# Performance work log

Hardware: AMD Instinct MI355X
Metric: run time of the kernel (lower is better)

The kernel has to match this reference:

```python
import jax, jax.numpy as jnp
import numpy as np

N, E, L = 50000, 300000, 4
DN, DE, H, DO = 11, 3, 128, 2


def _ln(x, g, b, eps=1e-5):
    m = jnp.mean(x, axis=-1, keepdims=True)
    v = jnp.mean((x - m) ** 2, axis=-1, keepdims=True)
    return (x - m) * jax.lax.rsqrt(v + eps) * g + b


def _mlp(x, w1, b1, w2, b2, g, be):
    # Linear -> ReLU -> Linear -> LayerNorm (matches torch Sequential)
    h = jax.nn.relu(x @ w1 + b1)
    return _ln(h @ w2 + b2, g, be)


def setup_inputs() -> dict:
    key = jax.random.key(0)
    ks = iter(jax.random.split(key, 64))
    def nrm(shape, s=1.0):
        return jax.random.normal(next(ks), shape, jnp.float32) * s
    w = 0.02  # weight init scale
    inp = {
        'x': nrm((N, DN)),
        'edge_index': jax.random.randint(next(ks), (2, E), 0, N, jnp.int32),
        'edge_attr': nrm((E, DE)),
        'mean_vec_x': nrm((DN,)),
        'std_vec_x': jnp.ones((DN,), jnp.float32),
        'mean_vec_edge': nrm((DE,)),
        'std_vec_edge': jnp.ones((DE,), jnp.float32),
        # node encoder
        'ne_w1': nrm((DN, H), w), 'ne_b1': jnp.zeros((H,), jnp.float32),
        'ne_w2': nrm((H, H), w), 'ne_b2': jnp.zeros((H,), jnp.float32),
        'ne_g': jnp.ones((H,), jnp.float32), 'ne_be': jnp.zeros((H,), jnp.float32),
        # edge encoder
        'ee_w1': nrm((DE, H), w), 'ee_b1': jnp.zeros((H,), jnp.float32),
        'ee_w2': nrm((H, H), w), 'ee_b2': jnp.zeros((H,), jnp.float32),
        'ee_g': jnp.ones((H,), jnp.float32), 'ee_be': jnp.zeros((H,), jnp.float32),
        # processor edge MLPs (stacked over L layers): Linear(3H->H), Linear(H->H), LN
        'pe_w1': nrm((L, 3 * H, H), w), 'pe_b1': jnp.zeros((L, H), jnp.float32),
        'pe_w2': nrm((L, H, H), w), 'pe_b2': jnp.zeros((L, H), jnp.float32),
        'pe_g': jnp.ones((L, H), jnp.float32), 'pe_be': jnp.zeros((L, H), jnp.float32),
        # processor node MLPs: Linear(2H->H), Linear(H->H), LN
        'pn_w1': nrm((L, 2 * H, H), w), 'pn_b1': jnp.zeros((L, H), jnp.float32),
        'pn_w2': nrm((L, H, H), w), 'pn_b2': jnp.zeros((L, H), jnp.float32),
        'pn_g': jnp.ones((L, H), jnp.float32), 'pn_be': jnp.zeros((L, H), jnp.float32),
        # decoder: Linear(H->H) ReLU Linear(H->DO)
        'de_w1': nrm((H, H), w), 'de_b1': jnp.zeros((H,), jnp.float32),
        'de_w2': nrm((H, DO), w), 'de_b2': jnp.zeros((DO,), jnp.float32),
    }
    return inp


def reference(x, edge_index, edge_attr, mean_vec_x, std_vec_x, mean_vec_edge, std_vec_edge,
              ne_w1, ne_b1, ne_w2, ne_b2, ne_g, ne_be,
              ee_w1, ee_b1, ee_w2, ee_b2, ee_g, ee_be,
              pe_w1, pe_b1, pe_w2, pe_b2, pe_g, pe_be,
              pn_w1, pn_b1, pn_w2, pn_b2, pn_g, pn_be,
              de_w1, de_b1, de_w2, de_b2):
    x = (x - mean_vec_x) / std_vec_x
    e = (edge_attr - mean_vec_edge) / std_vec_edge
    x = _mlp(x, ne_w1, ne_b1, ne_w2, ne_b2, ne_g, ne_be)   # [N, H]
    e = _mlp(e, ee_w1, ee_b1, ee_w2, ee_b2, ee_g, ee_be)   # [E, H]
    row, col = edge_index[0], edge_index[1]
    for i in range(L):
        # edge update: gather endpoints, concat with edge feature, residual
        msg_in = jnp.concatenate([x[row], x[col], e], axis=-1)  # [E, 3H]
        e = e + _mlp(msg_in, pe_w1[i], pe_b1[i], pe_w2[i], pe_b2[i], pe_g[i], pe_be[i])
        # aggregate messages (= updated edge_attr) at target nodes (col), sum-aggr
        agg = jax.ops.segment_sum(e, col, num_segments=N)       # [N, H]
        node_in = jnp.concatenate([x, agg], axis=-1)             # [N, 2H]
        x = x + _mlp(node_in, pn_w1[i], pn_b1[i], pn_w2[i], pn_b2[i], pn_g[i], pn_be[i])
    return jax.nn.relu(x @ de_w1 + de_b1) @ de_w2 + de_b2       # [N, DO]
```

## Files before the change

### kernel.cpp

```cpp
#include <hip/hip_runtime.h>
#include <hip/hip_bf16.h>


#define NN 50000
#define EE 300000

typedef unsigned int u32;
typedef unsigned short u16;
typedef __attribute__((ext_vector_type(8))) short bf16x8;
typedef __attribute__((ext_vector_type(4))) float f32x4;

__device__ __forceinline__ float bf2f(u16 v){ return __uint_as_float(((u32)v) << 16); }
__device__ __forceinline__ u16 f2bf(float f){
  u32 u = __float_as_uint(f);
  return (u16)((u + 0x7fffu + ((u >> 16) & 1u)) >> 16);
}
#define MFMA __builtin_amdgcn_mfma_f32_16x16x32_bf16

struct CD { const void* src; float* dst; int n; };
struct IngestArgs { CD d[34]; };

__global__ __launch_bounds__(256)
void ingest_kernel(IngestArgs a, const u32* __restrict__ probe) {
  const bool isbf = (probe[0] == 0x3F803F80u);
  const CD c = a.d[blockIdx.y];
  for (int i = blockIdx.x*256 + threadIdx.x; i < c.n; i += gridDim.x*256) {
    c.dst[i] = isbf ? bf2f(((const u16*)c.src)[i]) : ((const float*)c.src)[i];
  }
}

struct PackDesc { const float* src; u16* dst; int K; int Ksrc; };
struct PackArgs { PackDesc d[20]; };

__global__ __launch_bounds__(256)
void pack_b_kernel(PackArgs pa) {
  const PackDesc p = pa.d[blockIdx.y];
  const int total = (p.K >> 5) * 512;
  for (int idx = blockIdx.x*256 + threadIdx.x; idx < total; idx += gridDim.x*256) {
    const int lane = idx & 63;
    const int tile = idx >> 6;
    const int nt = tile & 7, kt = tile >> 3;
    const int col = nt*16 + (lane & 15);
    const int k0  = kt*32 + (lane >> 4) * 8;
    u32 w4[4];
    #pragma unroll
    for (int jj = 0; jj < 4; ++jj) {
      const int ka = k0 + 2*jj, kb = k0 + 2*jj + 1;
      const u16 lo = (ka < p.Ksrc) ? f2bf(p.src[(size_t)ka * 128 + col]) : (u16)0;
      const u16 hi = (kb < p.Ksrc) ? f2bf(p.src[(size_t)kb * 128 + col]) : (u16)0;
      w4[jj] = (u32)lo | ((u32)hi << 16);
    }
    *(uint4*)(p.dst + (size_t)idx * 8) = make_uint4(w4[0], w4[1], w4[2], w4[3]);
  }
}

__global__ __launch_bounds__(256)
void zero_kernel(int4* __restrict__ p, int n4) {
  for (int i = blockIdx.x*256 + threadIdx.x; i < n4; i += gridDim.x*256)
    p[i] = make_int4(0, 0, 0, 0);
}

__global__ __launch_bounds__(256)
void hist_kernel(const int* __restrict__ ei, int* __restrict__ deg) {
  for (int i = blockIdx.x*256 + threadIdx.x; i < EE; i += gridDim.x*256)
    atomicAdd(&deg[ei[EE + i]], 1);
}

__global__ __launch_bounds__(1024)
void scan_kernel(const int* __restrict__ deg, int* __restrict__ start,
                 int* __restrict__ cursor) {
  __shared__ int sums[1024];
  const int t = threadIdx.x;
  const int base = t * 49;
  int s = 0;
  for (int j = 0; j < 49; ++j) { const int i = base + j; if (i < NN) s += deg[i]; }
  sums[t] = s; __syncthreads();
  for (int off = 1; off < 1024; off <<= 1) {
    int v = (t >= off) ? sums[t - off] : 0;
    __syncthreads();
    sums[t] += v;
    __syncthreads();
  }
  int ex = (t == 0) ? 0 : sums[t - 1];
  for (int j = 0; j < 49; ++j) {
    const int i = base + j;
    if (i < NN) { start[i] = ex; cursor[i] = ex; ex += deg[i]; }
  }
  if (t == 1023) start[NN] = ex;
}

__global__ __launch_bounds__(256)
void scatter_kernel(const int* __restrict__ ei, int* __restrict__ cursor,
                    int* __restrict__ perm, int* __restrict__ src_p,
                    int* __restrict__ dst_p) {
  for (int i = blockIdx.x*256 + threadIdx.x; i < EE; i += gridDim.x*256) {
    const int c = ei[EE + i];
    const int pos = atomicAdd(&cursor[c], 1);
    perm[pos]  = i;
    src_p[pos] = ei[i];
    dst_p[pos] = c;
  }
}

template<int KIN, int MODE>
__global__ __launch_bounds__(256)
void enc_mfma(const u16* __restrict__ w1pk, const float* __restrict__ b1,
              const u16* __restrict__ w2pk, const float* __restrict__ b2,
              const float* __restrict__ g,  const float* __restrict__ be,
              const float* __restrict__ raw, const float* __restrict__ mean,
              const float* __restrict__ stdv, const int* __restrict__ perm,
              float* __restrict__ x, u16* __restrict__ outb, int nrows)
{
  constexpr int STR = 296;
  __shared__ u16 As[64 * STR];
  const int lane  = threadIdx.x & 63;
  const int wv    = threadIdx.x >> 6;
  const int col_l = lane & 15;
  const int quad  = lane >> 4;
  const int m0    = wv * 16;
  const int r0    = blockIdx.x * 64;

  for (int t = lane; t < 256; t += 64)
    ((u32*)As)[(m0 + (t >> 4)) * 148 + (t & 15)] = 0u;
  for (int t = lane; t < 16 * KIN; t += 64) {
    const int r = t / KIN, k = t - r * KIN;
    int srow = min(r0 + m0 + r, nrows - 1);
    if constexpr (MODE == 1) srow = perm[srow];
    const float v = (raw[(size_t)srow * KIN + k] - mean[k]) / stdv[k];
    As[(m0 + r) * STR + k] = f2bf(v);
  }

  float b1v[8], b2v[8], gv[8], bev[8];
  #pragma unroll
  for (int nt = 0; nt < 8; ++nt) {
    b1v[nt] = b1[nt*16 + col_l]; b2v[nt] = b2[nt*16 + col_l];
    gv[nt]  = g [nt*16 + col_l]; bev[nt] = be[nt*16 + col_l];
  }

  const f32x4 zf = {0.f, 0.f, 0.f, 0.f};
  const bf16x8* bq1 = (const bf16x8*)w1pk;
  const bf16x8* bq2 = (const bf16x8*)w2pk;
  const u16* arow = As + (size_t)(m0 + col_l) * STR + quad * 8;

  f32x4 acc[8];
  #pragma unroll
  for (int nt = 0; nt < 8; ++nt) acc[nt] = zf;
  {
    const bf16x8 af = *(const bf16x8*)(arow);
    #pragma unroll
    for (int nt = 0; nt < 8; ++nt)
      acc[nt] = MFMA(af, bq1[nt*64 + lane], acc[nt], 0, 0, 0);
  }
  #pragma unroll
  for (int nt = 0; nt < 8; ++nt) {
    #pragma unroll
    for (int rg = 0; rg < 4; ++rg) {
      const float hv = fmaxf(acc[nt][rg] + b1v[nt], 0.f);
      As[(size_t)(m0 + quad*4 + rg) * STR + 32 + nt*16 + col_l] = f2bf(hv);
    }
  }
  f32x4 acc2[8];
  #pragma unroll
  for (int nt = 0; nt < 8; ++nt) acc2[nt] = zf;
  #pragma unroll
  for (int kt = 0; kt < 4; ++kt) {
    const bf16x8 af = *(const bf16x8*)(arow + 32 + kt * 32);
    #pragma unroll
    for (int nt = 0; nt < 8; ++nt)
      acc2[nt] = MFMA(af, bq2[(kt*8+nt)*64 + lane], acc2[nt], 0, 0, 0);
  }
  #pragma unroll
  for (int rg = 0; rg < 4; ++rg) {
    float v[8];
    float s1 = 0.f, s2 = 0.f;
    #pragma unroll
    for (int nt = 0; nt < 8; ++nt) {
      v[nt] = acc2[nt][rg] + b2v[nt];
      s1 += v[nt]; s2 += v[nt]*v[nt];
    }
    #pragma unroll
    for (int off = 1; off < 16; off <<= 1) {
      s1 += __shfl_xor(s1, off);
      s2 += __shfl_xor(s2, off);
    }
    const float mu   = s1 * (1.f/128.f);
    const float var  = s2 * (1.f/128.f) - mu*mu;
    const float rstd = rsqrtf(var + 1e-5f);
    const int rloc = m0 + quad*4 + rg;
    const int row  = r0 + rloc;
    #pragma unroll
    for (int nt = 0; nt < 8; ++nt) {
      const float y = (v[nt] - mu) * rstd * gv[nt] + bev[nt];
      As[(size_t)rloc * STR + 160 + nt*16 + col_l] = f2bf(y);
      if (MODE == 0 && row < nrows) x[(size_t)row*128 + nt*16 + col_l] = y;
    }
  }
  #pragma unroll
  for (int r = 0; r < 16; ++r) {
    const int row = r0 + m0 + r;
    if (row < nrows)
      ((u32*)(outb + (size_t)row * 128))[lane] =
          ((const u32*)(As + (size_t)(m0 + r) * STR + 160))[lane];
  }
}

__global__ __launch_bounds__(512, 2)
void edge_mfma(const u16* __restrict__ w1pk, const float* __restrict__ b1,
               const u16* __restrict__ w2pk, const float* __restrict__ b2,
               const float* __restrict__ g, const float* __restrict__ be,
               const u16* __restrict__ xb, u16* __restrict__ eb,
               const int* __restrict__ src_p, const int* __restrict__ dst_p)
{
  extern __shared__ u16 lds[];
  u16* lw1 = lds;
  u16* lw2 = lds + 49152;
  u16* lh  = lds + 65536;

  const int lane = threadIdx.x & 63;
  const int wv   = threadIdx.x >> 6;
  const int m    = lane & 15;
  const int q    = lane >> 4;
  const int rbase = wv * 16;

  for (int i = threadIdx.x; i < 6144; i += 512)
    ((uint4*)lw1)[i] = ((const uint4*)w1pk)[i];
  for (int i = threadIdx.x; i < 2048; i += 512)
    ((uint4*)lw2)[i] = ((const uint4*)w2pk)[i];

  float b1v[8], b2v[8], gv[8], bev[8];
  #pragma unroll
  for (int nt = 0; nt < 8; ++nt) {
    b1v[nt] = b1[nt*16 + m]; b2v[nt] = b2[nt*16 + m];
    gv[nt]  = g [nt*16 + m]; bev[nt] = be[nt*16 + m];
  }
  __syncthreads();

  const int ntiles = (EE + 127) >> 7;
  bf16x8 A[12];

  auto loadA = [&](int t) {
    const int grow = min(t*128 + rbase + m, EE-1);
    const u16* p0 = xb + (size_t)src_p[grow] * 128 + q*8;
    const u16* p1 = xb + (size_t)dst_p[grow] * 128 + q*8;
    const u16* p2 = eb + (size_t)grow * 128 + q*8;
    #pragma unroll
    for (int kt = 0; kt < 4; ++kt) {
      A[kt]   = *(const bf16x8*)(p0 + kt*32);
      A[4+kt] = *(const bf16x8*)(p1 + kt*32);
      A[8+kt] = *(const bf16x8*)(p2 + kt*32);
    }
  };

  loadA(blockIdx.x);
  for (int t = blockIdx.x; t < ntiles; t += 256) {
    #pragma unroll
    for (int nt = 0; nt < 8; ++nt) {
      f32x4 c = {0.f,0.f,0.f,0.f};
      #pragma unroll
      for (int kt = 0; kt < 12; ++kt) {
        const bf16x8 bf = *(const bf16x8*)(lw1 + (size_t)(kt*8+nt)*512 + lane*8);
        c = MFMA(A[kt], bf, c, 0, 0, 0);
      }
      #pragma unroll
      for (int rg = 0; rg < 4; ++rg) {
        const float hv = fmaxf(c[rg] + b1v[nt], 0.f);
        const int row = rbase + q*4 + rg;
        const int col = nt*16 + m;
        lh[row*128 + (((col>>3) ^ (row&7))<<3) + (col&7)] = f2bf(hv);
      }
    }
    const int tn = t + 256;
    if (tn < ntiles) loadA(tn);
    f32x4 acc2[8];
    #pragma unroll
    for (int nt = 0; nt < 8; ++nt) acc2[nt] = {0.f,0.f,0.f,0.f};
    #pragma unroll
    for (int kt2 = 0; kt2 < 4; ++kt2) {
      const int ra = rbase + m;
      const bf16x8 h0 = *(const bf16x8*)(lh + ra*128 + (((kt2*4+q) ^ (ra&7))<<3));
      #pragma unroll
      for (int nt = 0; nt < 8; ++nt) {
        const bf16x8 bf = *(const bf16x8*)(lw2 + (size_t)(kt2*8+nt)*512 + lane*8);
        acc2[nt] = MFMA(h0, bf, acc2[nt], 0, 0, 0);
      }
    }
    #pragma unroll
    for (int rg = 0; rg < 4; ++rg) {
      const int rloc = q*4 + rg;
      const int grow = min(t*128 + rbase + rloc, EE-1);
      float v[8]; float s1 = 0.f, s2 = 0.f;
      #pragma unroll
      for (int nt = 0; nt < 8; ++nt) {
        v[nt] = acc2[nt][rg] + b2v[nt];
        s1 += v[nt]; s2 += v[nt]*v[nt];
      }
      #pragma unroll
      for (int off = 1; off < 16; off <<= 1) {
        s1 += __shfl_xor(s1, off);
        s2 += __shfl_xor(s2, off);
      }
      const float mu   = s1 * (1.f/128.f);
      const float rstd = rsqrtf(s2*(1.f/128.f) - mu*mu + 1e-5f);
      #pragma unroll
      for (int nt = 0; nt < 8; ++nt) {
        const float y  = (v[nt] - mu) * rstd * gv[nt] + bev[nt];
        const float eo = bf2f(eb[(size_t)grow*128 + nt*16 + m]);
        const int row = rbase + rloc;
        const int col = nt*16 + m;
        lh[row*128 + (((col>>3) ^ (row&7))<<3) + (col&7)] = f2bf(y + eo);
      }
    }
    #pragma unroll
    for (int r = 0; r < 16; ++r) {
      const int grow = t*128 + rbase + r;
      if (grow < EE) {
        const int ch = (lane >> 2) ^ (r & 7);
        ((u32*)(eb + (size_t)grow * 128))[lane] =
            *(const u32*)(lh + (rbase + r)*128 + (ch<<3) + 2*(lane & 3));
      }
    }
  }
}

__global__ __launch_bounds__(512, 2)
void node_mfma(const u16* __restrict__ w1pk, const float* __restrict__ b1,
               const u16* __restrict__ w2pk, const float* __restrict__ b2,
               const float* __restrict__ g, const float* __restrict__ be,
               float* __restrict__ x, u16* __restrict__ xb,
               const u16* __restrict__ eb, const int* __restrict__ start)
{
  extern __shared__ u16 lds[];
  u16* lw1 = lds;
  u16* lw2 = lds + 32768;
  u16* lh  = lds + 49152;
  u16* lag = lds + 65536;

  const int lane = threadIdx.x & 63;
  const int wv   = threadIdx.x >> 6;
  const int m    = lane & 15;
  const int q    = lane >> 4;
  const int rbase = wv * 16;

  for (int i = threadIdx.x; i < 4096; i += 512)
    ((uint4*)lw1)[i] = ((const uint4*)w1pk)[i];
  for (int i = threadIdx.x; i < 2048; i += 512)
    ((uint4*)lw2)[i] = ((const uint4*)w2pk)[i];

  float b1v[8], b2v[8], gv[8], bev[8];
  #pragma unroll
  for (int nt = 0; nt < 8; ++nt) {
    b1v[nt] = b1[nt*16 + m]; b2v[nt] = b2[nt*16 + m];
    gv[nt]  = g [nt*16 + m]; bev[nt] = be[nt*16 + m];
  }
  __syncthreads();

  const int ntiles = (NN + 127) >> 7;
  for (int t = blockIdx.x; t < ntiles; t += 256) {
    const int gbase = t*128 + rbase;
    const int sv = start[min(gbase + (lane & 31), NN)];
    for (int r = 0; r < 16; ++r) {
      const int s0 = __shfl(sv, r), s1 = __shfl(sv, r + 1);
      float a0 = 0.f, a1 = 0.f;
      int j = s0;
      for (; j + 4 <= s1; j += 4) {
        const u32 q0 = ((const u32*)(eb + (size_t)(j  ) * 128))[lane];
        const u32 q1 = ((const u32*)(eb + (size_t)(j+1) * 128))[lane];
        const u32 q2 = ((const u32*)(eb + (size_t)(j+2) * 128))[lane];
        const u32 q3 = ((const u32*)(eb + (size_t)(j+3) * 128))[lane];
        a0 += bf2f((u16)q0) + bf2f((u16)q1) + bf2f((u16)q2) + bf2f((u16)q3);
        a1 += bf2f((u16)(q0>>16)) + bf2f((u16)(q1>>16)) + bf2f((u16)(q2>>16)) + bf2f((u16)(q3>>16));
      }
      for (; j < s1; ++j) {
        const u32 qq = ((const u32*)(eb + (size_t)j * 128))[lane];
        a0 += bf2f((u16)qq); a1 += bf2f((u16)(qq>>16));
      }
      const int lr = rbase + r;
      const int ch = (lane >> 2) ^ (r & 7);
      *(u32*)(lag + lr*128 + (ch<<3) + 2*(lane & 3)) =
          (u32)f2bf(a0) | ((u32)f2bf(a1) << 16);
    }
    bf16x8 A[8];
    {
      const int grow = min(gbase + m, NN-1);
      const u16* p0 = xb + (size_t)grow * 128 + q*8;
      const int lr = rbase + m;
      #pragma unroll
      for (int kt = 0; kt < 4; ++kt) {
        A[kt]   = *(const bf16x8*)(p0 + kt*32);
        A[4+kt] = *(const bf16x8*)(lag + lr*128 + (((kt*4+q) ^ (m&7))<<3));
      }
    }
    #pragma unroll
    for (int nt = 0; nt < 8; ++nt) {
      f32x4 c = {0.f,0.f,0.f,0.f};
      #pragma unroll
      for (int kt = 0; kt < 8; ++kt) {
        const bf16x8 bf = *(const bf16x8*)(lw1 + (size_t)(kt*8+nt)*512 + lane*8);
        c = MFMA(A[kt], bf, c, 0, 0, 0);
      }
      #pragma unroll
      for (int rg = 0; rg < 4; ++rg) {
        const float hv = fmaxf(c[rg] + b1v[nt], 0.f);
        const int row = rbase + q*4 + rg;
        const int col = nt*16 + m;
        lh[row*128 + (((col>>3) ^ (row&7))<<3) + (col&7)] = f2bf(hv);
      }
    }
    f32x4 acc2[8];
    #pragma unroll
    for (int nt = 0; nt < 8; ++nt) acc2[nt] = {0.f,0.f,0.f,0.f};
    #pragma unroll
    for (int kt2 = 0; kt2 < 4; ++kt2) {
      const int ra = rbase + m;
      const bf16x8 h0 = *(const bf16x8*)(lh + ra*128 + (((kt2*4+q) ^ (ra&7))<<3));
      #pragma unroll
      for (int nt = 0; nt < 8; ++nt) {
        const bf16x8 bf = *(const bf16x8*)(lw2 + (size_t)(kt2*8+nt)*512 + lane*8);
        acc2[nt] = MFMA(h0, bf, acc2[nt], 0, 0, 0);
      }
    }
    #pragma unroll
    for (int rg = 0; rg < 4; ++rg) {
      const int rloc = q*4 + rg;
      const int grow = t*128 + rbase + rloc;
      const int growc = min(grow, NN-1);
      float v[8]; float s1 = 0.f, s2 = 0.f;
      #pragma unroll
      for (int nt = 0; nt < 8; ++nt) {
        v[nt] = acc2[nt][rg] + b2v[nt];
        s1 += v[nt]; s2 += v[nt]*v[nt];
      }
      #pragma unroll
      for (int off = 1; off < 16; off <<= 1) {
        s1 += __shfl_xor(s1, off);
        s2 += __shfl_xor(s2, off);
      }
      const float mu   = s1 * (1.f/128.f);
      const float rstd = rsqrtf(s2*(1.f/128.f) - mu*mu + 1e-5f);
      #pragma unroll
      for (int nt = 0; nt < 8; ++nt) {
        const float y  = (v[nt] - mu) * rstd * gv[nt] + bev[nt];
        const float xn = y + x[(size_t)growc*128 + nt*16 + m];
        if (grow < NN) x[(size_t)grow*128 + nt*16 + m] = xn;
        const int row = rbase + rloc;
        const int col = nt*16 + m;
        lh[row*128 + (((col>>3) ^ (row&7))<<3) + (col&7)] = f2bf(xn);
      }
    }
    #pragma unroll
    for (int r = 0; r < 16; ++r) {
      const int grow = t*128 + rbase + r;
      if (grow < NN) {
        const int ch = (lane >> 2) ^ (r & 7);
        ((u32*)(xb + (size_t)grow * 128))[lane] =
            *(const u32*)(lh + (rbase + r)*128 + (ch<<3) + 2*(lane & 3));
      }
    }
  }
}

constexpr int TM  = 8;
constexpr int WPB = 2;

__global__ __launch_bounds__(WPB*64)
void decoder_kernel(const float* __restrict__ x,
                    const float* __restrict__ w1, const float* __restrict__ b1,
                    const float* __restrict__ w2, const float* __restrict__ b2,
                    void* __restrict__ out, const u32* __restrict__ probe,
                    int nrows)
{
  const bool isbf = (probe[0] == 0x3F803F80u);
  const int lane = threadIdx.x & 63;
  const int wv   = threadIdx.x >> 6;
  const int wgl  = blockIdx.x * WPB + wv;
  const int nw   = gridDim.x * WPB;
  extern __shared__ float smem[];
  float* in_s = smem + wv * (TM * 128);

  const float2* w1p = ((const float2*)w1) + lane;
  const float b1l = b1[2*lane], b1h = b1[2*lane+1];
  const float2 wA = ((const float2*)w2)[2*lane];
  const float2 wB = ((const float2*)w2)[2*lane+1];
  const float c0 = b2[0], c1 = b2[1];

  for (int r0 = wgl * TM; r0 < nrows; r0 += nw * TM) {
    const int rcnt = min(TM, nrows - r0);
    for (int t = lane; t < rcnt * 128; t += 64) {
      const int r = t >> 7, k = t & 127;
      in_s[r*128 + k] = x[(size_t)(r0+r)*128 + k];
    }
    float a0[TM], a1[TM];
    #pragma unroll
    for (int r=0;r<TM;++r){ a0[r]=0.f; a1[r]=0.f; }
    for (int k = 0; k < 128; k += 2) {
      const float2 wa = w1p[(k  )*64];
      const float2 wb = w1p[(k+1)*64];
      #pragma unroll
      for (int r=0;r<TM;++r){
        const float2 av = *(const float2*)(in_s + r*128 + k);
        a0[r] = fmaf(av.x, wa.x, a0[r]); a1[r] = fmaf(av.x, wa.y, a1[r]);
        a0[r] = fmaf(av.y, wb.x, a0[r]); a1[r] = fmaf(av.y, wb.y, a1[r]);
      }
    }
    for (int r = 0; r < rcnt; ++r) {
      const float h0 = fmaxf(a0[r] + b1l, 0.f);
      const float h1 = fmaxf(a1[r] + b1h, 0.f);
      float p0 = fmaf(h0, wA.x, h1 * wB.x);
      float p1 = fmaf(h0, wA.y, h1 * wB.y);
      #pragma unroll
      for (int off = 32; off; off >>= 1) {
        p0 += __shfl_xor(p0, off);
        p1 += __shfl_xor(p1, off);
      }
      if (lane == 0) {
        const float o0 = p0 + c0;
        const float o1 = p1 + c1;
        if (isbf) ((u32*)out)[r0 + r] = (u32)f2bf(o0) | ((u32)f2bf(o1) << 16);
        else      *(float2*)((float*)out + (size_t)(r0 + r)*2) = make_float2(o0, o1);
      }
    }
  }
}

extern "C" void kernel_launch(void* const* d_in, const int* in_sizes, int n_in,
                              void* d_out, int out_size, void* d_ws, size_t ws_size,
                              hipStream_t stream) {
  static const int src_idx[34] = {0,2,3,4,5,6,
    7,8,9,10,11,12, 13,14,15,16,17,18,
    19,20,21,22,23,24, 25,26,27,28,29,30, 31,32,33,34};
  static const int sz[34] = {550000,900000,11,11,3,3,
    1408,128,16384,128,128,128,
    384,128,16384,128,128,128,
    196608,512,65536,512,512,512,
    131072,512,65536,512,512,512,
    16384,128,256,2};

  IngestArgs ia;
  const float* cp[35] = {};
  float* w = (float*)d_ws;
  for (int j = 0; j < 34; ++j) {
    ia.d[j].src = d_in[src_idx[j]];
    ia.d[j].dst = w;
    ia.d[j].n   = sz[j];
    cp[src_idx[j]] = w;
    w += sz[j];
  }
  w = (float*)(((uintptr_t)w + 63) & ~(uintptr_t)63);
  float* x   = w;
  u16*   xb  = (u16*)(x + (size_t)NN*128);
  u16*   e   = xb + (size_t)NN*128;
  u16*   pk  = e  + (size_t)EE*128;
  u16* pk_pe1 = pk;
  u16* pk_pe2 = pk_pe1 + (size_t)4*384*128;
  u16* pk_pn1 = pk_pe2 + (size_t)4*128*128;
  u16* pk_pn2 = pk_pn1 + (size_t)4*256*128;
  u16* pk_ne1 = pk_pn2 + (size_t)4*128*128;
  u16* pk_ne2 = pk_ne1 + (size_t)32*128;
  u16* pk_ee1 = pk_ne2 + (size_t)128*128;
  u16* pk_ee2 = pk_ee1 + (size_t)32*128;
  int* deg    = (int*)(pk_ee2 + (size_t)128*128);
  int* start  = deg + NN;
  int* cursor = start + NN + 1;
  int* perm   = cursor + NN;
  int* src_p  = perm + EE;
  int* dst_p  = src_p + EE;

  const u32* probe = (const u32*)d_in[4];
  const int* ei    = (const int*)d_in[1];

  hipFuncSetAttribute((const void*)edge_mfma,
                      hipFuncAttributeMaxDynamicSharedMemorySize, 163840);
  hipFuncSetAttribute((const void*)node_mfma,
                      hipFuncAttributeMaxDynamicSharedMemorySize, 163840);

  ingest_kernel<<<dim3(128, 34), 256, 0, stream>>>(ia, probe);

  PackArgs pa;
  for (int l = 0; l < 4; ++l) {
    pa.d[l*4+0] = { cp[19] + (size_t)l*384*128, pk_pe1 + (size_t)l*384*128, 384, 384 };
    pa.d[l*4+1] = { cp[21] + (size_t)l*128*128, pk_pe2 + (size_t)l*128*128, 128, 128 };
    pa.d[l*4+2] = { cp[25] + (size_t)l*256*128, pk_pn1 + (size_t)l*256*128, 256, 256 };
    pa.d[l*4+3] = { cp[27] + (size_t)l*128*128, pk_pn2 + (size_t)l*128*128, 128, 128 };
  }
  pa.d[16] = { cp[7],  pk_ne1,  32,  11 };
  pa.d[17] = { cp[9],  pk_ne2, 128, 128 };
  pa.d[18] = { cp[13], pk_ee1,  32,   3 };
  pa.d[19] = { cp[15], pk_ee2, 128, 128 };
  pack_b_kernel<<<dim3(24, 20), 256, 0, stream>>>(pa);

  zero_kernel<<<dim3(64), 256, 0, stream>>>((int4*)deg, NN/4);
  hist_kernel<<<dim3(512), 256, 0, stream>>>(ei, deg);
  scan_kernel<<<dim3(1), 1024, 0, stream>>>(deg, start, cursor);
  scatter_kernel<<<dim3(512), 256, 0, stream>>>(ei, cursor, perm, src_p, dst_p);

  enc_mfma<11, 0><<<dim3((NN + 63)/64), 256, 0, stream>>>(
      pk_ne1, cp[8], pk_ne2, cp[10], cp[11], cp[12],
      cp[0], cp[3], cp[4], nullptr, x, xb, NN);
  enc_mfma<3, 1><<<dim3((EE + 63)/64), 256, 0, stream>>>(
      pk_ee1, cp[14], pk_ee2, cp[16], cp[17], cp[18],
      cp[2], cp[5], cp[6], perm, nullptr, e, EE);

  for (int l = 0; l < 4; ++l) {
    edge_mfma<<<dim3(256), dim3(512), 163840, stream>>>(
        pk_pe1 + (size_t)l*384*128, cp[20] + l*128,
        pk_pe2 + (size_t)l*128*128, cp[22] + l*128,
        cp[23] + l*128, cp[24] + l*128,
        xb, e, src_p, dst_p);
    node_mfma<<<dim3(256), dim3(512), 163840, stream>>>(
        pk_pn1 + (size_t)l*256*128, cp[26] + l*128,
        pk_pn2 + (size_t)l*128*128, cp[28] + l*128,
        cp[29] + l*128, cp[30] + l*128,
        x, xb, e, start);
  }

  decoder_kernel<<<dim3((NN + TM*WPB - 1)/(TM*WPB)), dim3(WPB*64),
                   (size_t)(WPB*TM*128*4), stream>>>(
      x, cp[31], cp[32], cp[33], cp[34], d_out, probe, NN);
}
```

Before: 1.149 ms.

## Double-buffer edge tile loads and halve node tiles to eight rows per wave

The edge MLP kernel now holds two register buffers of gathered A operands and alternates tiles, so the next tile's gathers are issued before the current tile's compute. The residual edge read moves into the coalesced write-back loop, replacing the scattered per-element reads. The node kernel processes eight real rows per wave (64 per block) with padded MFMA rows, which doubles tile count to spread segment-sum work across more blocks, at the cost of half-wasted MFMA work and higher register pressure from the doubled A buffer.

```diff
diff --git a/kernel.cpp b/kernel.cpp
--- a/kernel.cpp
+++ b/kernel.cpp
@@ -236,30 +236,29 @@
   __syncthreads();
 
   const int ntiles = (EE + 127) >> 7;
-  bf16x8 A[12];
-
-  auto loadA = [&](int t) {
+  bf16x8 A[2][12];
+
+  auto loadA = [&](int t, int b) {
     const int grow = min(t*128 + rbase + m, EE-1);
     const u16* p0 = xb + (size_t)src_p[grow] * 128 + q*8;
     const u16* p1 = xb + (size_t)dst_p[grow] * 128 + q*8;
     const u16* p2 = eb + (size_t)grow * 128 + q*8;
     #pragma unroll
     for (int kt = 0; kt < 4; ++kt) {
-      A[kt]   = *(const bf16x8*)(p0 + kt*32);
-      A[4+kt] = *(const bf16x8*)(p1 + kt*32);
-      A[8+kt] = *(const bf16x8*)(p2 + kt*32);
+      A[b][kt]   = *(const bf16x8*)(p0 + kt*32);
+      A[b][4+kt] = *(const bf16x8*)(p1 + kt*32);
+      A[b][8+kt] = *(const bf16x8*)(p2 + kt*32);
     }
   };
 
-  loadA(blockIdx.x);
-  for (int t = blockIdx.x; t < ntiles; t += 256) {
+  auto compute = [&](int t, int b) {
     #pragma unroll
     for (int nt = 0; nt < 8; ++nt) {
       f32x4 c = {0.f,0.f,0.f,0.f};
       #pragma unroll
       for (int kt = 0; kt < 12; ++kt) {
         const bf16x8 bf = *(const bf16x8*)(lw1 + (size_t)(kt*8+nt)*512 + lane*8);
-        c = MFMA(A[kt], bf, c, 0, 0, 0);
+        c = MFMA(A[b][kt], bf, c, 0, 0, 0);
       }
       #pragma unroll
       for (int rg = 0; rg < 4; ++rg) {
@@ -269,8 +268,6 @@
         lh[row*128 + (((col>>3) ^ (row&7))<<3) + (col&7)] = f2bf(hv);
       }
     }
-    const int tn = t + 256;
-    if (tn < ntiles) loadA(tn);
     f32x4 acc2[8];
     #pragma unroll
     for (int nt = 0; nt < 8; ++nt) acc2[nt] = {0.f,0.f,0.f,0.f};
@@ -287,7 +284,6 @@
     #pragma unroll
     for (int rg = 0; rg < 4; ++rg) {
       const int rloc = q*4 + rg;
-      const int grow = min(t*128 + rbase + rloc, EE-1);
       float v[8]; float s1 = 0.f, s2 = 0.f;
       #pragma unroll
       for (int nt = 0; nt < 8; ++nt) {
@@ -303,21 +299,33 @@
       const float rstd = rsqrtf(s2*(1.f/128.f) - mu*mu + 1e-5f);
       #pragma unroll
       for (int nt = 0; nt < 8; ++nt) {
-        const float y  = (v[nt] - mu) * rstd * gv[nt] + bev[nt];
-        const float eo = bf2f(eb[(size_t)grow*128 + nt*16 + m]);
+        const float y = (v[nt] - mu) * rstd * gv[nt] + bev[nt];
         const int row = rbase + rloc;
         const int col = nt*16 + m;
-        lh[row*128 + (((col>>3) ^ (row&7))<<3) + (col&7)] = f2bf(y + eo);
+        lh[row*128 + (((col>>3) ^ (row&7))<<3) + (col&7)] = f2bf(y);
       }
     }
     #pragma unroll
     for (int r = 0; r < 16; ++r) {
       const int grow = t*128 + rbase + r;
       if (grow < EE) {
+        const u32 eo = ((const u32*)(eb + (size_t)grow * 128))[lane];
         const int ch = (lane >> 2) ^ (r & 7);
-        ((u32*)(eb + (size_t)grow * 128))[lane] =
-            *(const u32*)(lh + (rbase + r)*128 + (ch<<3) + 2*(lane & 3));
-      }
+        const u32 yv = *(const u32*)(lh + (rbase + r)*128 + (ch<<3) + 2*(lane & 3));
+        const float lo = bf2f((u16)eo) + bf2f((u16)yv);
+        const float hi = bf2f((u16)(eo >> 16)) + bf2f((u16)(yv >> 16));
+        ((u32*)(eb + (size_t)grow * 128))[lane] = (u32)f2bf(lo) | ((u32)f2bf(hi) << 16);
+      }
+    }
+  };
+
+  loadA(blockIdx.x, 0);
+  for (int t = blockIdx.x; t < ntiles; t += 512) {
+    if (t + 256 < ntiles) loadA(t + 256, 1);
+    compute(t, 0);
+    if (t + 256 < ntiles) {
+      if (t + 512 < ntiles) loadA(t + 512, 0);
+      compute(t + 256, 1);
     }
   }
 }
@@ -339,7 +347,7 @@
   const int wv   = threadIdx.x >> 6;
   const int m    = lane & 15;
   const int q    = lane >> 4;
-  const int rbase = wv * 16;
+  const int rl0  = wv * 16;
 
   for (int i = threadIdx.x; i < 4096; i += 512)
     ((uint4*)lw1)[i] = ((const uint4*)w1pk)[i];
@@ -354,11 +362,11 @@
   }
   __syncthreads();
 
-  const int ntiles = (NN + 127) >> 7;
+  const int ntiles = (NN + 63) >> 6;
   for (int t = blockIdx.x; t < ntiles; t += 256) {
-    const int gbase = t*128 + rbase;
-    const int sv = start[min(gbase + (lane & 31), NN)];
-    for (int r = 0; r < 16; ++r) {
+    const int gbase = t*64 + wv*8;
+    const int sv = start[min(gbase + (lane & 15), NN)];
+    for (int r = 0; r < 8; ++r) {
       const int s0 = __shfl(sv, r), s1 = __shfl(sv, r + 1);
       float a0 = 0.f, a1 = 0.f;
       int j = s0;
@@ -374,16 +382,16 @@
         const u32 qq = ((const u32*)(eb + (size_t)j * 128))[lane];
         a0 += bf2f((u16)qq); a1 += bf2f((u16)(qq>>16));
       }
-      const int lr = rbase + r;
+      const int lr = rl0 + r;
       const int ch = (lane >> 2) ^ (r & 7);
       *(u32*)(lag + lr*128 + (ch<<3) + 2*(lane & 3)) =
           (u32)f2bf(a0) | ((u32)f2bf(a1) << 16);
     }
     bf16x8 A[8];
     {
-      const int grow = min(gbase + m, NN-1);
+      const int grow = min(gbase + (m & 7), NN-1);
       const u16* p0 = xb + (size_t)grow * 128 + q*8;
-      const int lr = rbase + m;
+      const int lr = rl0 + m;
       #pragma unroll
       for (int kt = 0; kt < 4; ++kt) {
         A[kt]   = *(const bf16x8*)(p0 + kt*32);
@@ -401,7 +409,7 @@
       #pragma unroll
       for (int rg = 0; rg < 4; ++rg) {
         const float hv = fmaxf(c[rg] + b1v[nt], 0.f);
-        const int row = rbase + q*4 + rg;
+        const int row = rl0 + q*4 + rg;
         const int col = nt*16 + m;
         lh[row*128 + (((col>>3) ^ (row&7))<<3) + (col&7)] = f2bf(hv);
       }
@@ -411,7 +419,7 @@
     for (int nt = 0; nt < 8; ++nt) acc2[nt] = {0.f,0.f,0.f,0.f};
     #pragma unroll
     for (int kt2 = 0; kt2 < 4; ++kt2) {
-      const int ra = rbase + m;
+      const int ra = rl0 + m;
       const bf16x8 h0 = *(const bf16x8*)(lh + ra*128 + (((kt2*4+q) ^ (ra&7))<<3));
       #pragma unroll
       for (int nt = 0; nt < 8; ++nt) {
@@ -422,8 +430,8 @@
     #pragma unroll
     for (int rg = 0; rg < 4; ++rg) {
       const int rloc = q*4 + rg;
-      const int grow = t*128 + rbase + rloc;
-      const int growc = min(grow, NN-1);
+      const int grow = t*64 + wv*8 + rloc;
+      const int growc = min(min(grow, t*64 + wv*8 + 7), NN-1);
       float v[8]; float s1 = 0.f, s2 = 0.f;
       #pragma unroll
       for (int nt = 0; nt < 8; ++nt) {
@@ -437,23 +445,24 @@
       }
       const float mu   = s1 * (1.f/128.f);
       const float rstd = rsqrtf(s2*(1.f/128.f) - mu*mu + 1e-5f);
+      const bool real = (rloc < 8) && (grow < NN);
       #pragma unroll
       for (int nt = 0; nt < 8; ++nt) {
         const float y  = (v[nt] - mu) * rstd * gv[nt] + bev[nt];
         const float xn = y + x[(size_t)growc*128 + nt*16 + m];
-        if (grow < NN) x[(size_t)grow*128 + nt*16 + m] = xn;
-        const int row = rbase + rloc;
+        if (real) x[(size_t)grow*128 + nt*16 + m] = xn;
+        const int row = rl0 + rloc;
         const int col = nt*16 + m;
         lh[row*128 + (((col>>3) ^ (row&7))<<3) + (col&7)] = f2bf(xn);
       }
     }
     #pragma unroll
-    for (int r = 0; r < 16; ++r) {
-      const int grow = t*128 + rbase + r;
+    for (int r = 0; r < 8; ++r) {
+      const int grow = t*64 + wv*8 + r;
       if (grow < NN) {
         const int ch = (lane >> 2) ^ (r & 7);
         ((u32*)(xb + (size_t)grow * 128))[lane] =
-            *(const u32*)(lh + (rbase + r)*128 + (ch<<3) + 2*(lane & 3));
+            *(const u32*)(lh + (rl0 + r)*128 + (ch<<3) + 2*(lane & 3));
       }
     }
   }
```

After: 1.229 ms. 1.07x slower.

## Stream edge-MLP first-layer weights through double-buffered LDS to raise occupancy

Applied to the files above, without the earlier changes.

The edge kernel no longer keeps the full W1 and W2 resident in LDS. W1 is now streamed in four K-chunks through two small LDS buffers, with a barrier per chunk, and W2 plus the bias and LayerNorm vectors are read straight from global/L2. LDS drops to 80 KB and the grid doubles to 512 blocks with a launch bound of 4, so more waves can hide the gather latency. In exchange it adds per-tile barriers and repeated weight reloads from L2, and the residual add now happens at bf16 precision during the store.

```diff
diff --git a/kernel.cpp b/kernel.cpp
--- a/kernel.cpp
+++ b/kernel.cpp
@@ -204,7 +204,7 @@
   }
 }
 
-__global__ __launch_bounds__(512, 2)
+__global__ __launch_bounds__(512, 4)
 void edge_mfma(const u16* __restrict__ w1pk, const float* __restrict__ b1,
                const u16* __restrict__ w2pk, const float* __restrict__ b2,
                const float* __restrict__ g, const float* __restrict__ be,
@@ -212,28 +212,16 @@
                const int* __restrict__ src_p, const int* __restrict__ dst_p)
 {
   extern __shared__ u16 lds[];
-  u16* lw1 = lds;
-  u16* lw2 = lds + 49152;
-  u16* lh  = lds + 65536;
-
-  const int lane = threadIdx.x & 63;
-  const int wv   = threadIdx.x >> 6;
+  u16* wbuf0 = lds;
+  u16* wbuf1 = lds + 12288;
+  u16* lh    = lds + 24576;
+
+  const int tid  = threadIdx.x;
+  const int lane = tid & 63;
+  const int wv   = tid >> 6;
   const int m    = lane & 15;
   const int q    = lane >> 4;
   const int rbase = wv * 16;
-
-  for (int i = threadIdx.x; i < 6144; i += 512)
-    ((uint4*)lw1)[i] = ((const uint4*)w1pk)[i];
-  for (int i = threadIdx.x; i < 2048; i += 512)
-    ((uint4*)lw2)[i] = ((const uint4*)w2pk)[i];
-
-  float b1v[8], b2v[8], gv[8], bev[8];
-  #pragma unroll
-  for (int nt = 0; nt < 8; ++nt) {
-    b1v[nt] = b1[nt*16 + m]; b2v[nt] = b2[nt*16 + m];
-    gv[nt]  = g [nt*16 + m]; bev[nt] = be[nt*16 + m];
-  }
-  __syncthreads();
 
   const int ntiles = (EE + 127) >> 7;
   bf16x8 A[12];
@@ -251,47 +239,72 @@
     }
   };
 
+  {
+    const uint4* s = (const uint4*)w1pk;
+    uint4* d = (uint4*)wbuf0;
+    d[tid] = s[tid]; d[tid+512] = s[tid+512]; d[tid+1024] = s[tid+1024];
+  }
   loadA(blockIdx.x);
-  for (int t = blockIdx.x; t < ntiles; t += 256) {
+  __syncthreads();
+
+  for (int t = blockIdx.x; t < ntiles; t += 512) {
+    f32x4 c[8];
+    #pragma unroll
+    for (int nt = 0; nt < 8; ++nt) c[nt] = {0.f,0.f,0.f,0.f};
+    #pragma unroll
+    for (int ks = 0; ks < 4; ++ks) {
+      uint4 nx0, nx1, nx2;
+      {
+        const uint4* s = (const uint4*)w1pk + ((ks + 1) & 3) * 1536;
+        nx0 = s[tid]; nx1 = s[tid+512]; nx2 = s[tid+1024];
+      }
+      const u16* wb = (ks & 1) ? wbuf1 : wbuf0;
+      #pragma unroll
+      for (int nt = 0; nt < 8; ++nt) {
+        #pragma unroll
+        for (int ktl = 0; ktl < 3; ++ktl) {
+          const bf16x8 bf = *(const bf16x8*)(wb + (size_t)(ktl*8+nt)*512 + lane*8);
+          c[nt] = MFMA(A[ks*3+ktl], bf, c[nt], 0, 0, 0);
+        }
+      }
+      {
+        uint4* d = (uint4*)(((ks + 1) & 1) ? wbuf1 : wbuf0);
+        d[tid] = nx0; d[tid+512] = nx1; d[tid+1024] = nx2;
+      }
+      __syncthreads();
+    }
     #pragma unroll
     for (int nt = 0; nt < 8; ++nt) {
-      f32x4 c = {0.f,0.f,0.f,0.f};
-      #pragma unroll
-      for (int kt = 0; kt < 12; ++kt) {
-        const bf16x8 bf = *(const bf16x8*)(lw1 + (size_t)(kt*8+nt)*512 + lane*8);
-        c = MFMA(A[kt], bf, c, 0, 0, 0);
-      }
+      const float b1n = b1[nt*16 + m];
       #pragma unroll
       for (int rg = 0; rg < 4; ++rg) {
-        const float hv = fmaxf(c[rg] + b1v[nt], 0.f);
+        const float hv = fmaxf(c[nt][rg] + b1n, 0.f);
         const int row = rbase + q*4 + rg;
         const int col = nt*16 + m;
         lh[row*128 + (((col>>3) ^ (row&7))<<3) + (col&7)] = f2bf(hv);
       }
     }
-    const int tn = t + 256;
-    if (tn < ntiles) loadA(tn);
-    f32x4 acc2[8];
-    #pragma unroll
-    for (int nt = 0; nt < 8; ++nt) acc2[nt] = {0.f,0.f,0.f,0.f};
+    if (t + 512 < ntiles) loadA(t + 512);
+    f32x4 a2[8];
+    #pragma unroll
+    for (int nt = 0; nt < 8; ++nt) a2[nt] = {0.f,0.f,0.f,0.f};
     #pragma unroll
     for (int kt2 = 0; kt2 < 4; ++kt2) {
       const int ra = rbase + m;
       const bf16x8 h0 = *(const bf16x8*)(lh + ra*128 + (((kt2*4+q) ^ (ra&7))<<3));
       #pragma unroll
       for (int nt = 0; nt < 8; ++nt) {
-        const bf16x8 bf = *(const bf16x8*)(lw2 + (size_t)(kt2*8+nt)*512 + lane*8);
-        acc2[nt] = MFMA(h0, bf, acc2[nt], 0, 0, 0);
+        const bf16x8 bf = ((const bf16x8*)w2pk)[(kt2*8+nt)*64 + lane];
+        a2[nt] = MFMA(h0, bf, a2[nt], 0, 0, 0);
       }
     }
     #pragma unroll
     for (int rg = 0; rg < 4; ++rg) {
       const int rloc = q*4 + rg;
-      const int grow = min(t*128 + rbase + rloc, EE-1);
       float v[8]; float s1 = 0.f, s2 = 0.f;
       #pragma unroll
       for (int nt = 0; nt < 8; ++nt) {
-        v[nt] = acc2[nt][rg] + b2v[nt];
+        v[nt] = a2[nt][rg] + b2[nt*16 + m];
         s1 += v[nt]; s2 += v[nt]*v[nt];
       }
       #pragma unroll
@@ -303,20 +316,22 @@
       const float rstd = rsqrtf(s2*(1.f/128.f) - mu*mu + 1e-5f);
       #pragma unroll
       for (int nt = 0; nt < 8; ++nt) {
-        const float y  = (v[nt] - mu) * rstd * gv[nt] + bev[nt];
-        const float eo = bf2f(eb[(size_t)grow*128 + nt*16 + m]);
+        const float y = (v[nt] - mu) * rstd * g[nt*16 + m] + be[nt*16 + m];
         const int row = rbase + rloc;
         const int col = nt*16 + m;
-        lh[row*128 + (((col>>3) ^ (row&7))<<3) + (col&7)] = f2bf(y + eo);
+        lh[row*128 + (((col>>3) ^ (row&7))<<3) + (col&7)] = f2bf(y);
       }
     }
     #pragma unroll
     for (int r = 0; r < 16; ++r) {
       const int grow = t*128 + rbase + r;
       if (grow < EE) {
+        const u32 eo = ((const u32*)(eb + (size_t)grow * 128))[lane];
         const int ch = (lane >> 2) ^ (r & 7);
-        ((u32*)(eb + (size_t)grow * 128))[lane] =
-            *(const u32*)(lh + (rbase + r)*128 + (ch<<3) + 2*(lane & 3));
+        const u32 yv = *(const u32*)(lh + (rbase + r)*128 + (ch<<3) + 2*(lane & 3));
+        const float lo = bf2f((u16)eo) + bf2f((u16)yv);
+        const float hi = bf2f((u16)(eo >> 16)) + bf2f((u16)(yv >> 16));
+        ((u32*)(eb + (size_t)grow * 128))[lane] = (u32)f2bf(lo) | ((u32)f2bf(hi) << 16);
       }
     }
   }
@@ -569,7 +584,7 @@
   const int* ei    = (const int*)d_in[1];
 
   hipFuncSetAttribute((const void*)edge_mfma,
-                      hipFuncAttributeMaxDynamicSharedMemorySize, 163840);
+                      hipFuncAttributeMaxDynamicSharedMemorySize, 81920);
   hipFuncSetAttribute((const void*)node_mfma,
                       hipFuncAttributeMaxDynamicSharedMemorySize, 163840);
 
@@ -601,7 +616,7 @@
       cp[2], cp[5], cp[6], perm, nullptr, e, EE);
 
   for (int l = 0; l < 4; ++l) {
-    edge_mfma<<<dim3(256), dim3(512), 163840, stream>>>(
+    edge_mfma<<<dim3(512), dim3(512), 81920, stream>>>(
         pk_pe1 + (size_t)l*384*128, cp[20] + l*128,
         pk_pe2 + (size_t)l*128*128, cp[22] + l*128,
         cp[23] + l*128, cp[24] + l*128,
```

Result: slower. 2.770 ms (+141.0%).

## Process two 16-row halves per wave in edge MLP to reuse weight loads

Applied to the files above, without the earlier changes.

The edge MLP kernel now handles 256 edges per tile (32 rows per wave) instead of 128. Each LDS weight fragment of the first layer feeds two MFMAs, halving LDS weight reads per edge and exposing independent MFMA chains. The second half's hidden activations stay in registers while the first half runs through layer 2 and LayerNorm in the shared LDS buffer. The residual add is moved into a coalesced read-modify-write of the edge row. The cost is much higher register pressure (two A fragment sets for prefetch plus h1v), which may lower occupancy or cause spills.

```diff
diff --git a/kernel.cpp b/kernel.cpp
--- a/kernel.cpp
+++ b/kernel.cpp
@@ -235,89 +235,117 @@
   }
   __syncthreads();
 
-  const int ntiles = (EE + 127) >> 7;
-  bf16x8 A[12];
+  const int ntiles = (EE + 255) >> 8;
+  bf16x8 A[2][12];
 
   auto loadA = [&](int t) {
-    const int grow = min(t*128 + rbase + m, EE-1);
-    const u16* p0 = xb + (size_t)src_p[grow] * 128 + q*8;
-    const u16* p1 = xb + (size_t)dst_p[grow] * 128 + q*8;
-    const u16* p2 = eb + (size_t)grow * 128 + q*8;
-    #pragma unroll
-    for (int kt = 0; kt < 4; ++kt) {
-      A[kt]   = *(const bf16x8*)(p0 + kt*32);
-      A[4+kt] = *(const bf16x8*)(p1 + kt*32);
-      A[8+kt] = *(const bf16x8*)(p2 + kt*32);
+    #pragma unroll
+    for (int h = 0; h < 2; ++h) {
+      const int grow = min(t*256 + wv*32 + h*16 + m, EE-1);
+      const u16* p0 = xb + (size_t)src_p[grow] * 128 + q*8;
+      const u16* p1 = xb + (size_t)dst_p[grow] * 128 + q*8;
+      const u16* p2 = eb + (size_t)grow * 128 + q*8;
+      #pragma unroll
+      for (int kt = 0; kt < 4; ++kt) {
+        A[h][kt]   = *(const bf16x8*)(p0 + kt*32);
+        A[h][4+kt] = *(const bf16x8*)(p1 + kt*32);
+        A[h][8+kt] = *(const bf16x8*)(p2 + kt*32);
+      }
+    }
+  };
+
+  auto tail_half = [&](f32x4* a2, int gbase) {
+    #pragma unroll
+    for (int kt2 = 0; kt2 < 4; ++kt2) {
+      const int ra = rbase + m;
+      const bf16x8 h0 = *(const bf16x8*)(lh + ra*128 + (((kt2*4+q) ^ (ra&7))<<3));
+      #pragma unroll
+      for (int nt = 0; nt < 8; ++nt) {
+        const bf16x8 bf = *(const bf16x8*)(lw2 + (size_t)(kt2*8+nt)*512 + lane*8);
+        a2[nt] = MFMA(h0, bf, a2[nt], 0, 0, 0);
+      }
+    }
+    #pragma unroll
+    for (int rg = 0; rg < 4; ++rg) {
+      const int rloc = q*4 + rg;
+      float v[8]; float s1 = 0.f, s2 = 0.f;
+      #pragma unroll
+      for (int nt = 0; nt < 8; ++nt) {
+        v[nt] = a2[nt][rg] + b2v[nt];
+        s1 += v[nt]; s2 += v[nt]*v[nt];
+      }
+      #pragma unroll
+      for (int off = 1; off < 16; off <<= 1) {
+        s1 += __shfl_xor(s1, off);
+        s2 += __shfl_xor(s2, off);
+      }
+      const float mu   = s1 * (1.f/128.f);
+      const float rstd = rsqrtf(s2*(1.f/128.f) - mu*mu + 1e-5f);
+      #pragma unroll
+      for (int nt = 0; nt < 8; ++nt) {
+        const float y = (v[nt] - mu) * rstd * gv[nt] + bev[nt];
+        const int row = rbase + rloc;
+        const int col = nt*16 + m;
+        lh[row*128 + (((col>>3) ^ (row&7))<<3) + (col&7)] = f2bf(y);
+      }
+    }
+    #pragma unroll
+    for (int r = 0; r < 16; ++r) {
+      const int grow = gbase + r;
+      if (grow < EE) {
+        const u32 eo = ((const u32*)(eb + (size_t)grow * 128))[lane];
+        const int ch = (lane >> 2) ^ (r & 7);
+        const u32 yv = *(const u32*)(lh + (rbase + r)*128 + (ch<<3) + 2*(lane & 3));
+        const float lo = bf2f((u16)eo) + bf2f((u16)yv);
+        const float hi = bf2f((u16)(eo >> 16)) + bf2f((u16)(yv >> 16));
+        ((u32*)(eb + (size_t)grow * 128))[lane] = (u32)f2bf(lo) | ((u32)f2bf(hi) << 16);
+      }
     }
   };
 
   loadA(blockIdx.x);
   for (int t = blockIdx.x; t < ntiles; t += 256) {
+    const int gbase = t*256 + wv*32;
+    float h1v[8][4];
     #pragma unroll
     for (int nt = 0; nt < 8; ++nt) {
-      f32x4 c = {0.f,0.f,0.f,0.f};
+      f32x4 c0 = {0.f,0.f,0.f,0.f}, c1 = {0.f,0.f,0.f,0.f};
       #pragma unroll
       for (int kt = 0; kt < 12; ++kt) {
         const bf16x8 bf = *(const bf16x8*)(lw1 + (size_t)(kt*8+nt)*512 + lane*8);
-        c = MFMA(A[kt], bf, c, 0, 0, 0);
+        c0 = MFMA(A[0][kt], bf, c0, 0, 0, 0);
+        c1 = MFMA(A[1][kt], bf, c1, 0, 0, 0);
       }
       #pragma unroll
       for (int rg = 0; rg < 4; ++rg) {
-        const float hv = fmaxf(c[rg] + b1v[nt], 0.f);
+        const float hv = fmaxf(c0[rg] + b1v[nt], 0.f);
         const int row = rbase + q*4 + rg;
         const int col = nt*16 + m;
         lh[row*128 + (((col>>3) ^ (row&7))<<3) + (col&7)] = f2bf(hv);
-      }
-    }
-    const int tn = t + 256;
-    if (tn < ntiles) loadA(tn);
-    f32x4 acc2[8];
-    #pragma unroll
-    for (int nt = 0; nt < 8; ++nt) acc2[nt] = {0.f,0.f,0.f,0.f};
-    #pragma unroll
-    for (int kt2 = 0; kt2 < 4; ++kt2) {
-      const int ra = rbase + m;
-      const bf16x8 h0 = *(const bf16x8*)(lh + ra*128 + (((kt2*4+q) ^ (ra&7))<<3));
-      #pragma unroll
-      for (int nt = 0; nt < 8; ++nt) {
-        const bf16x8 bf = *(const bf16x8*)(lw2 + (size_t)(kt2*8+nt)*512 + lane*8);
-        acc2[nt] = MFMA(h0, bf, acc2[nt], 0, 0, 0);
-      }
-    }
-    #pragma unroll
-    for (int rg = 0; rg < 4; ++rg) {
-      const int rloc = q*4 + rg;
-      const int grow = min(t*128 + rbase + rloc, EE-1);
-      float v[8]; float s1 = 0.f, s2 = 0.f;
-      #pragma unroll
-      for (int nt = 0; nt < 8; ++nt) {
-        v[nt] = acc2[nt][rg] + b2v[nt];
-        s1 += v[nt]; s2 += v[nt]*v[nt];
-      }
-      #pragma unroll
-      for (int off = 1; off < 16; off <<= 1) {
-        s1 += __shfl_xor(s1, off);
-        s2 += __shfl_xor(s2, off);
-      }
-      const float mu   = s1 * (1.f/128.f);
-      const float rstd = rsqrtf(s2*(1.f/128.f) - mu*mu + 1e-5f);
-      #pragma unroll
-      for (int nt = 0; nt < 8; ++nt) {
-        const float y  = (v[nt] - mu) * rstd * gv[nt] + bev[nt];
-        const float eo = bf2f(eb[(size_t)grow*128 + nt*16 + m]);
-        const int row = rbase + rloc;
+        h1v[nt][rg] = fmaxf(c1[rg] + b1v[nt], 0.f);
+      }
+    }
+    if (t + 256 < ntiles) loadA(t + 256);
+    {
+      f32x4 a2[8];
+      #pragma unroll
+      for (int nt = 0; nt < 8; ++nt) a2[nt] = {0.f,0.f,0.f,0.f};
+      tail_half(a2, gbase);
+    }
+    #pragma unroll
+    for (int nt = 0; nt < 8; ++nt) {
+      #pragma unroll
+      for (int rg = 0; rg < 4; ++rg) {
+        const int row = rbase + q*4 + rg;
         const int col = nt*16 + m;
-        lh[row*128 + (((col>>3) ^ (row&7))<<3) + (col&7)] = f2bf(y + eo);
-      }
-    }
-    #pragma unroll
-    for (int r = 0; r < 16; ++r) {
-      const int grow = t*128 + rbase + r;
-      if (grow < EE) {
-        const int ch = (lane >> 2) ^ (r & 7);
-        ((u32*)(eb + (size_t)grow * 128))[lane] =
-            *(const u32*)(lh + (rbase + r)*128 + (ch<<3) + 2*(lane & 3));
-      }
+        lh[row*128 + (((col>>3) ^ (row&7))<<3) + (col&7)] = f2bf(h1v[nt][rg]);
+      }
+    }
+    {
+      f32x4 a2[8];
+      #pragma unroll
+      for (int nt = 0; nt < 8; ++nt) a2[nt] = {0.f,0.f,0.f,0.f};
+      tail_half(a2, gbase + 16);
     }
   }
 }
```

Result: slower. 1.504 ms (+30.9%).
